# Kernel optimization log

Measured on AMD Instinct MI355X. Metric: run time of the kernel, lower is better.

## Reference

```python
import jax, jax.numpy as jnp
import numpy as np
from jax import lax

NUM_MELS = 80
NQ = 256          # num_quants
WIN = 1024
HOP = 256
K_UP = 800        # upsample kernel
PAD_UP = K_UP + 4 * HOP - WIN   # = 800
RC = 120          # residual_channels
SC = 240          # skip_channels
KC = 2            # causal kernel
NB = 16           # num blocks
DILS = [1, 2, 4, 8, 16, 32, 64, 128] * 2
DN = ('NCH', 'OIH', 'NCH')


def conv1x1(x, w, b):
    # x: [B,C,T], w: [O,C], b: [O]
    return jnp.einsum('bct,oc->bot', x, w) + b[None, :, None]


def causal_conv(x, w, b, d):
    # x: [B,RC,T], w: [2RC,RC,KC], left-pad by d*(KC-1) -> causal, same length
    y = lax.conv_general_dilated(x, w, (1,), [(d * (KC - 1), 0)],
                                 rhs_dilation=(d,), dimension_numbers=DN)
    return y + b[None, :, None]


def setup_inputs() -> dict:
    key = jax.random.key(0)
    ks = jax.random.split(key, 20)
    s = 0.05
    n = jax.random.normal
    return {
        'waveforms': n(ks[0], (1, 40960), jnp.float32),
        'melspecs': n(ks[1], (1, NUM_MELS, 160), jnp.float32),
        # ConvTranspose-equivalent upsample weight, stored as direct conv weight [O,I,K]
        'up_w': s * n(ks[2], (NUM_MELS, NUM_MELS, K_UP), jnp.float32),
        'up_b': jnp.zeros((NUM_MELS,), jnp.float32),
        'in_w': s * n(ks[3], (RC, 1), jnp.float32),
        'in_b': jnp.zeros((RC,), jnp.float32),
        'blk_causal_w': s * n(ks[4], (NB, 2 * RC, RC, KC), jnp.float32),
        'blk_causal_b': jnp.zeros((NB, 2 * RC), jnp.float32),
        'blk_cond_w': s * n(ks[5], (NB, 2 * RC, NUM_MELS), jnp.float32),
        'blk_cond_b': jnp.zeros((NB, 2 * RC), jnp.float32),
        'blk_skip_w': s * n(ks[6], (NB, SC, RC), jnp.float32),
        'blk_skip_b': jnp.zeros((NB, SC), jnp.float32),
        'blk_res_w': s * n(ks[7], (NB, RC, RC), jnp.float32),
        'blk_res_b': jnp.zeros((NB, RC), jnp.float32),
        'h1_w': s * n(ks[8], (NQ, SC), jnp.float32),
        'h1_b': jnp.zeros((NQ,), jnp.float32),
        'h2_w': s * n(ks[9], (NQ, NQ), jnp.float32),
        'h2_b': jnp.zeros((NQ,), jnp.float32),
    }


def _forward(waveforms, melspecs, up_w, up_b, in_w, in_b,
             blk_causal_w, blk_causal_b, blk_cond_w, blk_cond_b,
             blk_skip_w, blk_skip_b, blk_res_w, blk_res_b,
             h1_w, h1_b, h2_w, h2_b):
    # ConvTranspose1d(stride=HOP, padding=PAD_UP) as lhs-dilated conv:
    # out_len = (F-1)*HOP + K_UP - 2*PAD_UP
    cond = lax.conv_general_dilated(
        melspecs, up_w, (1,), [(K_UP - 1 - PAD_UP, K_UP - 1 - PAD_UP)],
        lhs_dilation=(HOP,), dimension_numbers=DN) + up_b[None, :, None]
    L = min(waveforms.shape[-1], cond.shape[-1])
    wav = waveforms[..., :L]
    cond = cond[..., :L]

    res = conv1x1(wav[:, None, :], in_w, in_b)          # [B,RC,L]
    skip_sum = jnp.zeros((res.shape[0], SC, L), res.dtype)
    for i, d in enumerate(DILS):
        z = causal_conv(res, blk_causal_w[i], blk_causal_b[i], d) \
            + conv1x1(cond, blk_cond_w[i], blk_cond_b[i])  # [B,2RC,L]
        h = jnp.tanh(z[:, :RC]) * jax.nn.sigmoid(z[:, RC:])
        skip_sum = skip_sum + conv1x1(h, blk_skip_w[i], blk_skip_b[i])
        res = res + conv1x1(h, blk_res_w[i], blk_res_b[i])

    x = jax.nn.relu(skip_sum)
    x = jax.nn.relu(conv1x1(x, h1_w, h1_b))
    logits = conv1x1(x, h2_w, h2_b)                      # [B,NQ,L]
    return logits


def reference(waveforms, melspecs, up_w, up_b, in_w, in_b,
              blk_causal_w, blk_causal_b, blk_cond_w, blk_cond_b,
              blk_skip_w, blk_skip_b, blk_res_w, blk_res_b,
              h1_w, h1_b, h2_w, h2_b):
    return _forward(waveforms, melspecs, up_w, up_b, in_w, in_b,
                    blk_causal_w, blk_causal_b, blk_cond_w, blk_cond_b,
                    blk_skip_w, blk_skip_b, blk_res_w, blk_res_b,
                    h1_w, h1_b, h2_w, h2_b)
```

## Files before the change

### kernel.cpp

```cpp
#include <hip/hip_runtime.h>

#define L_LEN 39904
#define NT 624
#define RCH 120
#define SCH 240
#define CMEL 80
#define NQO 256
#define NBLK 16
#define KUP 800

typedef unsigned short u16;
typedef __attribute__((ext_vector_type(8))) short short8;
typedef __attribute__((ext_vector_type(4))) float f32x4;

#define MFMA(a, b, c) __builtin_amdgcn_mfma_f32_16x16x32_bf16((a), (b), (c), 0, 0, 0)

__device__ __forceinline__ u16 f2bf(float f) {
    unsigned u = __float_as_uint(f);
    u += 0x7FFFu + ((u >> 16) & 1u);
    return (u16)(u >> 16);
}
__device__ __forceinline__ unsigned pack2(float a, float b) {
    return (unsigned)f2bf(a) | ((unsigned)f2bf(b) << 16);
}
__device__ __forceinline__ float b16tof(u16 h) {
    return __uint_as_float((unsigned)h << 16);
}
__device__ __forceinline__ float gate(float a, float b) {
    float ea = __expf(2.f * a);
    float th = 1.f - 2.f * __builtin_amdgcn_rcpf(ea + 1.f);
    float sg = __builtin_amdgcn_rcpf(1.f + __expf(-b));
    return th * sg;
}

constexpr size_t O_CONDT = 0;
constexpr size_t O_RESA  = O_CONDT + 7023104;
constexpr size_t O_RESB  = O_RESA + 19153920;
constexpr size_t O_SKIP  = O_RESB + 19153920;
constexpr size_t O_ZFRAG = O_SKIP + 19153920;
constexpr size_t O_SKF   = O_ZFRAG + 2621440;
constexpr size_t O_RF    = O_SKF + 1048576;
constexpr size_t O_H1F   = O_RF + 524288;
constexpr size_t O_H2F   = O_H1F + 131072;
constexpr size_t O_UPF   = O_H2F + 131072;
constexpr size_t O_ZB    = O_UPF + 13107200;
constexpr size_t O_SKB   = O_ZB + 16384;

constexpr size_t H2_CONDT = 0;
constexpr size_t H2_RESF  = 7023104;
constexpr size_t H2_BFA   = H2_RESF + 19153920;
constexpr size_t H2_BFB   = H2_BFA + 9576960;
constexpr size_t H2_ZFRAG = H2_BFB + 9576960;
constexpr size_t H2_SKF   = H2_ZFRAG + 2621440;
constexpr size_t H2_RF    = H2_SKF + 1048576;
constexpr size_t H2_H1F   = H2_RF + 524288;
constexpr size_t H2_H2F   = H2_H1F + 131072;
constexpr size_t H2_ZB    = H2_H2F + 131072;
constexpr size_t H2_SKBS  = H2_ZB + 16384;
constexpr size_t H2_HALL  = H2_SKBS + 16384;
constexpr size_t H_BYTES  = (size_t)NBLK * L_LEN * 120 * 2;
constexpr size_t UPF_BYTES = 13107200;
constexpr size_t NEED_H = H2_HALL + (H_BYTES > UPF_BYTES ? H_BYTES : UPF_BYTES);

__global__ void k_prep_zfrag(const float* __restrict__ bc_w, const float* __restrict__ bq_w,
                             u16* __restrict__ dst) {
    int i = blockIdx.x * 256 + threadIdx.x;
    if (i >= NBLK * 10 * 16 * 512) return;
    int jj = i & 7, lane = (i >> 3) & 63, mt = (i >> 9) & 15;
    int rest = i >> 13, ks = rest % 10, blk = rest / 10;
    int m = mt * 16 + (lane & 15);
    int k = ks * 32 + ((lane >> 4) << 3) + jj;
    float v = 0.f;
    if (m < 240) {
        int o = (m & 1) ? (m >> 1) + 120 : (m >> 1);
        if (k < 120)       v = bc_w[((size_t)(blk * 240 + o) * 120 + k) * 2 + 0];
        else if (k < 240)  v = bc_w[((size_t)(blk * 240 + o) * 120 + (k - 120)) * 2 + 1];
        else               v = bq_w[(size_t)(blk * 240 + o) * 80 + (k - 240)];
    }
    dst[i] = f2bf(v);
}
__global__ void k_prep_skfrag(const float* __restrict__ bs_w, u16* __restrict__ dst) {
    int i = blockIdx.x * 256 + threadIdx.x;
    if (i >= NBLK * 4 * 16 * 512) return;
    int jj = i & 7, lane = (i >> 3) & 63, mt = (i >> 9) & 15;
    int rest = i >> 13, ks = rest & 3, blk = rest >> 2;
    int m = mt * 16 + (lane & 15);
    int k = ks * 32 + ((lane >> 4) << 3) + jj;
    float v = (m < 240 && k < 120) ? bs_w[(size_t)(blk * 240 + m) * 120 + k] : 0.f;
    dst[i] = f2bf(v);
}
__global__ void k_prep_rfrag(const float* __restrict__ br_w, u16* __restrict__ dst) {
    int i = blockIdx.x * 256 + threadIdx.x;
    if (i >= NBLK * 4 * 8 * 512) return;
    int jj = i & 7, lane = (i >> 3) & 63, mt = (i >> 9) & 7;
    int rest = i >> 12, ks = rest & 3, blk = rest >> 2;
    int m = mt * 16 + (lane & 15);
    int k = ks * 32 + ((lane >> 4) << 3) + jj;
    float v = (m < 120 && k < 120) ? br_w[(size_t)(blk * 120 + m) * 120 + k] : 0.f;
    dst[i] = f2bf(v);
}
__global__ void k_prep_h1frag(const float* __restrict__ h1_w, u16* __restrict__ dst) {
    int i = blockIdx.x * 256 + threadIdx.x;
    if (i >= 8 * 16 * 512) return;
    int jj = i & 7, lane = (i >> 3) & 63, mt = (i >> 9) & 15, ks = i >> 13;
    int m = mt * 16 + (lane & 15);
    int k = ks * 32 + ((lane >> 4) << 3) + jj;
    float v = (k < 240) ? h1_w[(size_t)m * 240 + k] : 0.f;
    dst[i] = f2bf(v);
}
__global__ void k_prep_h2frag(const float* __restrict__ h2_w, u16* __restrict__ dst) {
    int i = blockIdx.x * 256 + threadIdx.x;
    if (i >= 8 * 16 * 512) return;
    int jj = i & 7, lane = (i >> 3) & 63, mt = (i >> 9) & 15, ks = i >> 13;
    int m = mt * 16 + (lane & 15);
    int k = ks * 32 + ((lane >> 4) << 3) + jj;
    dst[i] = f2bf(h2_w[(size_t)m * 256 + k]);
}
__global__ void k_prep_upfrag(const float* __restrict__ up_w, u16* __restrict__ dst) {
    int i = blockIdx.x * 256 + threadIdx.x;
    if (i >= 256 * 10 * 5 * 512) return;
    int jj = i & 7, lane = (i >> 3) & 63;
    int rest = i >> 9;
    int mt = rest % 5; rest /= 5;
    int ks = rest % 10; int p = rest / 10;
    int m = mt * 16 + (lane & 15);
    int k = ks * 32 + ((lane >> 4) << 3) + jj;
    int c = k >> 2, j = k & 3;
    int r = (256 - ((p + 1) & 255)) & 255;
    int kk = r + 256 * j;
    float v = (m < 80 && kk < KUP) ? up_w[((size_t)m * 80 + c) * KUP + kk] : 0.f;
    dst[i] = f2bf(v);
}
__global__ void k_prep_zbias(const float* __restrict__ bc_b, const float* __restrict__ bq_b,
                             float* __restrict__ dst) {
    int i = blockIdx.x * 256 + threadIdx.x;
    if (i >= NBLK * 256) return;
    int m = i & 255, blk = i >> 8;
    float v = 0.f;
    if (m < 240) {
        int o = (m & 1) ? (m >> 1) + 120 : (m >> 1);
        v = bc_b[blk * 240 + o] + bq_b[blk * 240 + o];
    }
    dst[i] = v;
}
__global__ void k_prep_skbias(const float* __restrict__ bs_b, float* __restrict__ dst) {
    int i = blockIdx.x * 256 + threadIdx.x;
    if (i >= NBLK * 240) return;
    dst[i] = bs_b[i];
}
__global__ void k_prep_skbsum(const float* __restrict__ bs_b, float* __restrict__ dst) {
    int m = blockIdx.x * 256 + threadIdx.x;
    if (m >= 240) return;
    float s = 0.f;
    for (int i = 0; i < NBLK; i++) s += bs_b[i * 240 + m];
    dst[m] = s;
}
__global__ void k_res_initT(const float* __restrict__ wav, const float* __restrict__ in_w,
                            const float* __restrict__ in_b, float* __restrict__ resT) {
    int i = blockIdx.x * 256 + threadIdx.x;
    if (i >= L_LEN * RCH) return;
    int t = i / RCH, c = i % RCH;
    resT[i] = wav[t] * in_w[c] + in_b[c];
}
__global__ void k_res_initT2(const float* __restrict__ wav, const float* __restrict__ in_w,
                             const float* __restrict__ in_b, float* __restrict__ resT,
                             u16* __restrict__ resB) {
    int i = blockIdx.x * 256 + threadIdx.x;
    if (i >= L_LEN * RCH) return;
    int t = i / RCH, c = i % RCH;
    float v = wav[t] * in_w[c] + in_b[c];
    resT[i] = v;
    resB[i] = f2bf(v);
}

__global__ __launch_bounds__(256) void k_up(const float* __restrict__ mel,
        const u16* __restrict__ upf, const float* __restrict__ up_b,
        u16* __restrict__ condT) {
    __shared__ u16 s_ms[64 * 328];
    const int tid = threadIdx.x, l = tid & 63, w = tid >> 6;
    const int quad = l >> 4, tloc = l & 15;
    const int p = blockIdx.x, s0 = blockIdx.y * 64;
    for (int rr = 0; rr < 16; rr++) {
        int tt = w + 4 * rr;
        int sg = s0 + tt;
        #pragma unroll
        for (int base = 0; base < 320; base += 64) {
            int ck = base + l;
            int c = ck >> 2, j = ck & 3;
            int mi = 1 + j + sg;
            float v = (mi < 160) ? mel[c * 160 + mi] : 0.f;
            s_ms[tt * 328 + ck] = f2bf(v);
        }
    }
    __syncthreads();
    f32x4 acc[2][4];
    #pragma unroll
    for (int i = 0; i < 2; i++)
        #pragma unroll
        for (int n = 0; n < 4; n++) acc[i][n] = (f32x4){0.f, 0.f, 0.f, 0.f};
    const int nmt = (w == 0) ? 2 : 1;
    int mts[2]; mts[0] = w; mts[1] = 4;
    for (int ks = 0; ks < 10; ks++) {
        short8 b[4];
        int k0 = ks * 32 + quad * 8;
        #pragma unroll
        for (int n = 0; n < 4; n++)
            b[n] = *(const short8*)&s_ms[(n * 16 + tloc) * 328 + k0];
        const short8* ap = (const short8*)(upf) + ((size_t)p * 10 + ks) * 5 * 64;
        for (int i = 0; i < nmt; i++) {
            short8 a = ap[mts[i] * 64 + l];
            #pragma unroll
            for (int n = 0; n < 4; n++) acc[i][n] = MFMA(a, b[n], acc[i][n]);
        }
    }
    for (int i = 0; i < nmt; i++) {
        int o_base = mts[i] * 16 + quad * 4;
        float4 ub = *(const float4*)(up_b + o_base);
        float bb[4] = {ub.x, ub.y, ub.z, ub.w};
        #pragma unroll
        for (int n = 0; n < 4; n++) {
            int sg = s0 + n * 16 + tloc;
            int t = p + 256 * sg;
            if (t < L_LEN) {
                #pragma unroll
                for (int r = 0; r < 4; r++)
                    condT[(size_t)t * 88 + o_base + r] = f2bf(acc[i][n][r] + bb[r]);
            }
        }
    }
}

__global__ __launch_bounds__(512, 4) void k_block(
        const u16* __restrict__ condT, const float* __restrict__ resT_in,
        float* __restrict__ resT_out, u16* __restrict__ skipT,
        const u16* __restrict__ zfrag, const u16* __restrict__ skfrag,
        const u16* __restrict__ rfrag, const float* __restrict__ zbias,
        const float* __restrict__ skbias, const float* __restrict__ resb,
        int blk, int dil, int first) {
    __shared__ u16 s_x[64 * 328];
    u16* s_h = s_x;
    const int tid = threadIdx.x, l = tid & 63, w = tid >> 6;
    const int quad = l >> 4, tloc = l & 15;
    const int t0 = blockIdx.x * 64;
    const short8* zap = (const short8*)(zfrag) + (size_t)blk * 10 * 16 * 64;
    short8 a_cur[2], a_nxt[2];
    #pragma unroll
    for (int i = 0; i < 2; i++) a_cur[i] = zap[(size_t)(w * 2 + i) * 64 + l];
    for (int rr = 0; rr < 8; rr++) {
        int tt = w + 8 * rr;
        int tg = t0 + tt, tp = tg - dil;
        if (l < 60) {
            float2 pv = make_float2(0.f, 0.f), cv = make_float2(0.f, 0.f);
            if (tp >= 0 && tp < L_LEN) pv = *(const float2*)(resT_in + (size_t)tp * 120 + 2 * l);
            if (tg < L_LEN)            cv = *(const float2*)(resT_in + (size_t)tg * 120 + 2 * l);
            *(unsigned*)&s_x[tt * 328 + 2 * l]       = pack2(pv.x, pv.y);
            *(unsigned*)&s_x[tt * 328 + 120 + 2 * l] = pack2(cv.x, cv.y);
        }
        if (l < 40) {
            unsigned q = 0;
            if (tg < L_LEN) q = *(const unsigned*)(condT + (size_t)tg * 88 + 2 * l);
            *(unsigned*)&s_x[tt * 328 + 240 + 2 * l] = q;
        }
    }
    __syncthreads();
    f32x4 acc[2][4];
    #pragma unroll
    for (int i = 0; i < 2; i++)
        #pragma unroll
        for (int n = 0; n < 4; n++) acc[i][n] = (f32x4){0.f, 0.f, 0.f, 0.f};
    for (int ks = 0; ks < 10; ks++) {
        if (ks < 9) {
            #pragma unroll
            for (int i = 0; i < 2; i++)
                a_nxt[i] = zap[((size_t)(ks + 1) * 16 + w * 2 + i) * 64 + l];
        }
        int k0 = ks * 32 + quad * 8;
        short8 b[4];
        #pragma unroll
        for (int n = 0; n < 4; n++)
            b[n] = *(const short8*)&s_x[(n * 16 + tloc) * 328 + k0];
        #pragma unroll
        for (int i = 0; i < 2; i++)
            #pragma unroll
            for (int n = 0; n < 4; n++) acc[i][n] = MFMA(a_cur[i], b[n], acc[i][n]);
        #pragma unroll
        for (int i = 0; i < 2; i++) a_cur[i] = a_nxt[i];
    }
    const short8* sap = (const short8*)(skfrag) + (size_t)blk * 4 * 16 * 64;
    const short8* rap = (const short8*)(rfrag) + (size_t)blk * 4 * 8 * 64;
    short8 sa_c[2], sa_n[2], ra_c, ra_n;
    #pragma unroll
    for (int i = 0; i < 2; i++) sa_c[i] = sap[(size_t)(w * 2 + i) * 64 + l];
    ra_c = rap[(size_t)w * 64 + l];
    uint2 skp[2][4];
    if (!first) {
        #pragma unroll
        for (int i = 0; i < 2; i++) {
            int m_base = (w * 2 + i) * 16 + quad * 4;
            if (m_base < 240) {
                #pragma unroll
                for (int n = 0; n < 4; n++) {
                    int t = t0 + n * 16 + tloc;
                    if (t < L_LEN)
                        skp[i][n] = *(const uint2*)(skipT + (size_t)t * 240 + m_base);
                }
            }
        }
    }
    unsigned hu[2][4];
    #pragma unroll
    for (int i = 0; i < 2; i++) {
        int m_base = (w * 2 + i) * 16 + quad * 4;
        float4 bz4 = *(const float4*)(zbias + blk * 256 + m_base);
        #pragma unroll
        for (int n = 0; n < 4; n++) {
            float h0 = gate(acc[i][n][0] + bz4.x, acc[i][n][1] + bz4.y);
            float h1 = gate(acc[i][n][2] + bz4.z, acc[i][n][3] + bz4.w);
            hu[i][n] = pack2(h0, h1);
        }
    }
    __syncthreads();
    #pragma unroll
    for (int i = 0; i < 2; i++) {
        int j0 = (w * 2 + i) * 8 + quad * 2;
        #pragma unroll
        for (int n = 0; n < 4; n++)
            *(unsigned*)&s_h[(n * 16 + tloc) * 136 + j0] = hu[i][n];
    }
    __syncthreads();
    f32x4 sacc[2][4], racc[4];
    #pragma unroll
    for (int i = 0; i < 2; i++)
        #pragma unroll
        for (int n = 0; n < 4; n++) sacc[i][n] = (f32x4){0.f, 0.f, 0.f, 0.f};
    #pragma unroll
    for (int n = 0; n < 4; n++) racc[n] = (f32x4){0.f, 0.f, 0.f, 0.f};
    for (int ks = 0; ks < 4; ks++) {
        if (ks < 3) {
            #pragma unroll
            for (int i = 0; i < 2; i++)
                sa_n[i] = sap[((size_t)(ks + 1) * 16 + w * 2 + i) * 64 + l];
            ra_n = rap[((size_t)(ks + 1) * 8 + w) * 64 + l];
        }
        short8 b[4];
        int k0 = ks * 32 + quad * 8;
        #pragma unroll
        for (int n = 0; n < 4; n++)
            b[n] = *(const short8*)&s_h[(n * 16 + tloc) * 136 + k0];
        #pragma unroll
        for (int i = 0; i < 2; i++)
            #pragma unroll
            for (int n = 0; n < 4; n++) sacc[i][n] = MFMA(sa_c[i], b[n], sacc[i][n]);
        #pragma unroll
        for (int n = 0; n < 4; n++) racc[n] = MFMA(ra_c, b[n], racc[n]);
        #pragma unroll
        for (int i = 0; i < 2; i++) sa_c[i] = sa_n[i];
        ra_c = ra_n;
    }
    #pragma unroll
    for (int i = 0; i < 2; i++) {
        int m_base = (w * 2 + i) * 16 + quad * 4;
        if (m_base >= 240) continue;
        float4 sb4 = *(const float4*)(skbias + blk * 240 + m_base);
        #pragma unroll
        for (int n = 0; n < 4; n++) {
            int t = t0 + n * 16 + tloc;
            if (t >= L_LEN) continue;
            float x0 = sacc[i][n][0] + sb4.x;
            float x1 = sacc[i][n][1] + sb4.y;
            float x2 = sacc[i][n][2] + sb4.z;
            float x3 = sacc[i][n][3] + sb4.w;
            if (!first) {
                uint2 pv = skp[i][n];
                x0 += b16tof((u16)(pv.x & 0xFFFF));
                x1 += b16tof((u16)(pv.x >> 16));
                x2 += b16tof((u16)(pv.y & 0xFFFF));
                x3 += b16tof((u16)(pv.y >> 16));
            }
            uint2 ov;
            ov.x = pack2(x0, x1);
            ov.y = pack2(x2, x3);
            *(uint2*)(skipT + (size_t)t * 240 + m_base) = ov;
        }
    }
    {
        int m_base = w * 16 + quad * 4;
        if (m_base < 120) {
            float4 rb4 = *(const float4*)(resb + blk * 120 + m_base);
            #pragma unroll
            for (int n = 0; n < 4; n++) {
                int t = t0 + n * 16 + tloc;
                if (t >= L_LEN) continue;
                float4 cur = *(const float4*)(resT_in + (size_t)t * 120 + m_base);
                float4 o;
                o.x = cur.x + racc[n][0] + rb4.x;
                o.y = cur.y + racc[n][1] + rb4.y;
                o.z = cur.z + racc[n][2] + rb4.z;
                o.w = cur.w + racc[n][3] + rb4.w;
                *(float4*)(resT_out + (size_t)t * 120 + m_base) = o;
            }
        }
    }
}

__global__ __launch_bounds__(512, 4) void k_block_h2(
        const u16* __restrict__ condT, float* __restrict__ resF,
        const u16* __restrict__ bfIn, u16* __restrict__ bfOut,
        u16* __restrict__ hout,
        const u16* __restrict__ zfrag, const u16* __restrict__ rfrag,
        const float* __restrict__ zbias, const float* __restrict__ resb,
        int blk, int dil) {
    __shared__ u16 s_h[64 * 136];
    const int tid = threadIdx.x, l = tid & 63, w = tid >> 6;
    const int quad = l >> 4, tloc = l & 15;
    const int t0 = blockIdx.x * 64;
    const short8 ZV = {0, 0, 0, 0, 0, 0, 0, 0};
    int oP[4], oC[4], oQ[4];
    bool pz[4];
    #pragma unroll
    for (int n = 0; n < 4; n++) {
        int tn = t0 + n * 16 + tloc;
        int tc = tn < L_LEN ? tn : L_LEN - 1;
        int tp = tn - dil;
        pz[n] = (tp < 0);
        int tpc = tp < 0 ? 0 : (tp < L_LEN ? tp : L_LEN - 1);
        oP[n] = tpc * 120;
        oC[n] = tc * 120;
        oQ[n] = tc * 88;
    }
    const short8* zap = (const short8*)(zfrag) + (size_t)blk * 10 * 16 * 64;
    short8 a_cur[2], a_nxt[2];
    a_cur[0] = zap[(size_t)(w * 2 + 0) * 64 + l];
    a_cur[1] = zap[(size_t)(w * 2 + 1) * 64 + l];
    f32x4 acc[2][4];
    #pragma unroll
    for (int i = 0; i < 2; i++)
        #pragma unroll
        for (int n = 0; n < 4; n++) acc[i][n] = (f32x4){0.f, 0.f, 0.f, 0.f};
    short8 bc[4], bn[4];
    {
        int k0 = quad * 8;
        #pragma unroll
        for (int n = 0; n < 4; n++) {
            short8 v = *(const short8*)(bfIn + oP[n] + k0);
            if (pz[n]) v = ZV;
            bc[n] = v;
        }
    }
    #pragma unroll
    for (int ks = 0; ks < 10; ks++) {
        if (ks < 9) {
            int k1 = (ks + 1) * 32 + quad * 8;
            #pragma unroll
            for (int n = 0; n < 4; n++) {
                short8 v;
                if (k1 < 120) {
                    v = *(const short8*)(bfIn + oP[n] + k1);
                    if (pz[n]) v = ZV;
                } else if (k1 < 240) {
                    v = *(const short8*)(bfIn + oC[n] + (k1 - 120));
                } else {
                    v = *(const short8*)(condT + oQ[n] + (k1 - 240));
                }
                bn[n] = v;
            }
            a_nxt[0] = zap[((size_t)(ks + 1) * 16 + w * 2 + 0) * 64 + l];
            a_nxt[1] = zap[((size_t)(ks + 1) * 16 + w * 2 + 1) * 64 + l];
        }
        #pragma unroll
        for (int i = 0; i < 2; i++)
            #pragma unroll
            for (int n = 0; n < 4; n++) acc[i][n] = MFMA(a_cur[i], bc[n], acc[i][n]);
        #pragma unroll
        for (int n = 0; n < 4; n++) bc[n] = bn[n];
        a_cur[0] = a_nxt[0]; a_cur[1] = a_nxt[1];
    }
    const short8* rap = (const short8*)(rfrag) + (size_t)blk * 4 * 8 * 64;
    short8 ra_c = rap[(size_t)w * 64 + l], ra_n;
    const int m_r = w * 16 + quad * 4;
    float4 cur_pf[4] = {};
    if (m_r < 120) {
        #pragma unroll
        for (int n = 0; n < 4; n++) {
            int t = t0 + n * 16 + tloc;
            if (t < L_LEN) cur_pf[n] = *(const float4*)(resF + (size_t)t * 120 + m_r);
        }
    }
    unsigned hu[2][4];
    #pragma unroll
    for (int i = 0; i < 2; i++) {
        int m_base = (w * 2 + i) * 16 + quad * 4;
        float4 bz4 = *(const float4*)(zbias + blk * 256 + m_base);
        #pragma unroll
        for (int n = 0; n < 4; n++) {
            float h0 = gate(acc[i][n][0] + bz4.x, acc[i][n][1] + bz4.y);
            float h1 = gate(acc[i][n][2] + bz4.z, acc[i][n][3] + bz4.w);
            hu[i][n] = pack2(h0, h1);
        }
    }
    #pragma unroll
    for (int i = 0; i < 2; i++) {
        int j0 = (w * 2 + i) * 8 + quad * 2;
        #pragma unroll
        for (int n = 0; n < 4; n++)
            *(unsigned*)&s_h[(n * 16 + tloc) * 136 + j0] = hu[i][n];
    }
    __syncthreads();
    for (int rr = 0; rr < 8; rr++) {
        int tt = w + 8 * rr, tg = t0 + tt;
        if (l < 60 && tg < L_LEN)
            *(unsigned*)&hout[(size_t)tg * 120 + 2 * l] =
                *(const unsigned*)&s_h[tt * 136 + 2 * l];
    }
    f32x4 racc[4];
    #pragma unroll
    for (int n = 0; n < 4; n++) racc[n] = (f32x4){0.f, 0.f, 0.f, 0.f};
    for (int ks = 0; ks < 4; ks++) {
        if (ks < 3) ra_n = rap[((size_t)(ks + 1) * 8 + w) * 64 + l];
        short8 b[4];
        int k0 = ks * 32 + quad * 8;
        #pragma unroll
        for (int n = 0; n < 4; n++)
            b[n] = *(const short8*)&s_h[(n * 16 + tloc) * 136 + k0];
        #pragma unroll
        for (int n = 0; n < 4; n++) racc[n] = MFMA(ra_c, b[n], racc[n]);
        ra_c = ra_n;
    }
    if (m_r < 120) {
        float4 rb4 = *(const float4*)(resb + blk * 120 + m_r);
        #pragma unroll
        for (int n = 0; n < 4; n++) {
            int t = t0 + n * 16 + tloc;
            if (t >= L_LEN) continue;
            float4 o;
            o.x = cur_pf[n].x + racc[n][0] + rb4.x;
            o.y = cur_pf[n].y + racc[n][1] + rb4.y;
            o.z = cur_pf[n].z + racc[n][2] + rb4.z;
            o.w = cur_pf[n].w + racc[n][3] + rb4.w;
            *(float4*)(resF + (size_t)t * 120 + m_r) = o;
            uint2 hv;
            hv.x = pack2(o.x, o.y);
            hv.y = pack2(o.z, o.w);
            *(uint2*)(bfOut + (size_t)t * 120 + m_r) = hv;
        }
    }
}

__global__ __launch_bounds__(512, 4) void k_final(const u16* __restrict__ skipT,
        const u16* __restrict__ h1f, const u16* __restrict__ h2f,
        const float* __restrict__ h1_b, const float* __restrict__ h2_b,
        float* __restrict__ out) {
    __shared__ u16 s_m[64 * 264];
    const int tid = threadIdx.x, l = tid & 63, w = tid >> 6;
    const int quad = l >> 4, tloc = l & 15;
    const int t0 = blockIdx.x * 64;
    const short8* ap1 = (const short8*)h1f;
    short8 a_cur[2], a_nxt[2];
    #pragma unroll
    for (int i = 0; i < 2; i++) a_cur[i] = ap1[(size_t)(w * 2 + i) * 64 + l];
    for (int rr = 0; rr < 8; rr++) {
        int tt = w + 8 * rr;
        int tg = t0 + tt;
        uint2 v = make_uint2(0u, 0u);
        if (l < 60 && tg < L_LEN)
            v = *(const uint2*)(skipT + (size_t)tg * 240 + 4 * l);
        float x0 = fmaxf(b16tof((u16)(v.x & 0xFFFF)), 0.f);
        float x1 = fmaxf(b16tof((u16)(v.x >> 16)), 0.f);
        float x2 = fmaxf(b16tof((u16)(v.y & 0xFFFF)), 0.f);
        float x3 = fmaxf(b16tof((u16)(v.y >> 16)), 0.f);
        uint2 ov;
        ov.x = pack2(x0, x1);
        ov.y = pack2(x2, x3);
        *(uint2*)&s_m[tt * 264 + 4 * l] = ov;
    }
    __syncthreads();
    f32x4 acc[2][4];
    #pragma unroll
    for (int i = 0; i < 2; i++)
        #pragma unroll
        for (int n = 0; n < 4; n++) acc[i][n] = (f32x4){0.f, 0.f, 0.f, 0.f};
    for (int ks = 0; ks < 8; ks++) {
        if (ks < 7) {
            #pragma unroll
            for (int i = 0; i < 2; i++)
                a_nxt[i] = ap1[((size_t)(ks + 1) * 16 + w * 2 + i) * 64 + l];
        }
        short8 b[4];
        int k0 = ks * 32 + quad * 8;
        #pragma unroll
        for (int n = 0; n < 4; n++)
            b[n] = *(const short8*)&s_m[(n * 16 + tloc) * 264 + k0];
        #pragma unroll
        for (int i = 0; i < 2; i++)
            #pragma unroll
            for (int n = 0; n < 4; n++) acc[i][n] = MFMA(a_cur[i], b[n], acc[i][n]);
        #pragma unroll
        for (int i = 0; i < 2; i++) a_cur[i] = a_nxt[i];
    }
    unsigned ylo[2][4], yhi[2][4];
    #pragma unroll
    for (int i = 0; i < 2; i++) {
        int m_base = (w * 2 + i) * 16 + quad * 4;
        float4 b1 = *(const float4*)(h1_b + m_base);
        #pragma unroll
        for (int n = 0; n < 4; n++) {
            float y0 = fmaxf(acc[i][n][0] + b1.x, 0.f);
            float y1v = fmaxf(acc[i][n][1] + b1.y, 0.f);
            float y2 = fmaxf(acc[i][n][2] + b1.z, 0.f);
            float y3 = fmaxf(acc[i][n][3] + b1.w, 0.f);
            ylo[i][n] = pack2(y0, y1v);
            yhi[i][n] = pack2(y2, y3);
        }
    }
    const short8* ap2 = (const short8*)h2f;
    #pragma unroll
    for (int i = 0; i < 2; i++) a_cur[i] = ap2[(size_t)(w * 2 + i) * 64 + l];
    __syncthreads();
    #pragma unroll
    for (int i = 0; i < 2; i++) {
        int m_base = (w * 2 + i) * 16 + quad * 4;
        #pragma unroll
        for (int n = 0; n < 4; n++) {
            int t = n * 16 + tloc;
            *(unsigned*)&s_m[t * 264 + m_base]     = ylo[i][n];
            *(unsigned*)&s_m[t * 264 + m_base + 2] = yhi[i][n];
        }
    }
    __syncthreads();
    #pragma unroll
    for (int i = 0; i < 2; i++)
        #pragma unroll
        for (int n = 0; n < 4; n++) acc[i][n] = (f32x4){0.f, 0.f, 0.f, 0.f};
    for (int ks = 0; ks < 8; ks++) {
        if (ks < 7) {
            #pragma unroll
            for (int i = 0; i < 2; i++)
                a_nxt[i] = ap2[((size_t)(ks + 1) * 16 + w * 2 + i) * 64 + l];
        }
        short8 b[4];
        int k0 = ks * 32 + quad * 8;
        #pragma unroll
        for (int n = 0; n < 4; n++)
            b[n] = *(const short8*)&s_m[(n * 16 + tloc) * 264 + k0];
        #pragma unroll
        for (int i = 0; i < 2; i++)
            #pragma unroll
            for (int n = 0; n < 4; n++) acc[i][n] = MFMA(a_cur[i], b[n], acc[i][n]);
        #pragma unroll
        for (int i = 0; i < 2; i++) a_cur[i] = a_nxt[i];
    }
    #pragma unroll
    for (int i = 0; i < 2; i++) {
        int m_base = (w * 2 + i) * 16 + quad * 4;
        float4 b2 = *(const float4*)(h2_b + m_base);
        float bb[4] = {b2.x, b2.y, b2.z, b2.w};
        #pragma unroll
        for (int n = 0; n < 4; n++) {
            int t = t0 + n * 16 + tloc;
            if (t >= L_LEN) continue;
            #pragma unroll
            for (int r = 0; r < 4; r++)
                out[(size_t)(m_base + r) * L_LEN + t] = acc[i][n][r] + bb[r];
        }
    }
}

__global__ __launch_bounds__(512, 4) void k_final_h2(const u16* __restrict__ hall,
        const u16* __restrict__ skf, const u16* __restrict__ h1f,
        const u16* __restrict__ h2f, const float* __restrict__ skbsum,
        const float* __restrict__ h1_b, const float* __restrict__ h2_b,
        float* __restrict__ out) {
    __shared__ u16 s_m[64 * 264];
    const int tid = threadIdx.x, l = tid & 63, w = tid >> 6;
    const int quad = l >> 4, tloc = l & 15;
    const int t0 = blockIdx.x * 64;
    const short8 ZV = {0, 0, 0, 0, 0, 0, 0, 0};
    int ro[4];
    #pragma unroll
    for (int n = 0; n < 4; n++) {
        int tn = t0 + n * 16 + tloc;
        ro[n] = (tn < L_LEN ? tn : L_LEN - 1) * 120;
    }
    const bool kpad = (quad == 3);
    const int k0q = quad * 8;
    const short8* sap = (const short8*)skf;
    short8 sa_c[2], sa_n[2];
    sa_c[0] = sap[(size_t)(w * 2 + 0) * 64 + l];
    sa_c[1] = sap[(size_t)(w * 2 + 1) * 64 + l];
    f32x4 sacc[2][4];
    #pragma unroll
    for (int i = 0; i < 2; i++)
        #pragma unroll
        for (int n = 0; n < 4; n++) sacc[i][n] = (f32x4){0.f, 0.f, 0.f, 0.f};
    short8 bc[4], bn[4];
    #pragma unroll
    for (int n = 0; n < 4; n++)
        bc[n] = *(const short8*)(hall + ro[n] + k0q);
    for (int g = 0; g < 64; g++) {
        if (g < 63) {
            int g1 = g + 1;
            const u16* hp = hall + (size_t)(g1 >> 2) * ((size_t)L_LEN * 120);
            int kk = (g1 & 3) * 32 + k0q;
            bool pad = ((g1 & 3) == 3) && kpad;
            #pragma unroll
            for (int n = 0; n < 4; n++) {
                short8 v = *(const short8*)(hp + ro[n] + kk);
                if (pad) v = ZV;
                bn[n] = v;
            }
            sa_n[0] = sap[((size_t)g1 * 16 + w * 2 + 0) * 64 + l];
            sa_n[1] = sap[((size_t)g1 * 16 + w * 2 + 1) * 64 + l];
        }
        #pragma unroll
        for (int i2 = 0; i2 < 2; i2++)
            #pragma unroll
            for (int n = 0; n < 4; n++)
                sacc[i2][n] = MFMA(sa_c[i2], bc[n], sacc[i2][n]);
        #pragma unroll
        for (int n = 0; n < 4; n++) bc[n] = bn[n];
        sa_c[0] = sa_n[0]; sa_c[1] = sa_n[1];
    }
    const short8* ap1 = (const short8*)h1f;
    short8 a_cur[2], a_nxt[2];
    a_cur[0] = ap1[(size_t)(w * 2 + 0) * 64 + l];
    a_cur[1] = ap1[(size_t)(w * 2 + 1) * 64 + l];
    #pragma unroll
    for (int i2 = 0; i2 < 2; i2++) {
        int m_base = (w * 2 + i2) * 16 + quad * 4;
        float4 sb4 = make_float4(0.f, 0.f, 0.f, 0.f);
        bool valid = (m_base < 240);
        if (valid) sb4 = *(const float4*)(skbsum + m_base);
        #pragma unroll
        for (int n = 0; n < 4; n++) {
            float x0 = 0.f, x1 = 0.f, x2 = 0.f, x3 = 0.f;
            if (valid) {
                x0 = fmaxf(sacc[i2][n][0] + sb4.x, 0.f);
                x1 = fmaxf(sacc[i2][n][1] + sb4.y, 0.f);
                x2 = fmaxf(sacc[i2][n][2] + sb4.z, 0.f);
                x3 = fmaxf(sacc[i2][n][3] + sb4.w, 0.f);
            }
            int t = n * 16 + tloc;
            *(unsigned*)&s_m[t * 264 + m_base]     = pack2(x0, x1);
            *(unsigned*)&s_m[t * 264 + m_base + 2] = pack2(x2, x3);
        }
    }
    __syncthreads();
    f32x4 acc[2][4];
    #pragma unroll
    for (int i = 0; i < 2; i++)
        #pragma unroll
        for (int n = 0; n < 4; n++) acc[i][n] = (f32x4){0.f, 0.f, 0.f, 0.f};
    for (int ks = 0; ks < 8; ks++) {
        if (ks < 7) {
            #pragma unroll
            for (int i = 0; i < 2; i++)
                a_nxt[i] = ap1[((size_t)(ks + 1) * 16 + w * 2 + i) * 64 + l];
        }
        short8 b[4];
        int k0 = ks * 32 + quad * 8;
        #pragma unroll
        for (int n = 0; n < 4; n++)
            b[n] = *(const short8*)&s_m[(n * 16 + tloc) * 264 + k0];
        #pragma unroll
        for (int i = 0; i < 2; i++)
            #pragma unroll
            for (int n = 0; n < 4; n++) acc[i][n] = MFMA(a_cur[i], b[n], acc[i][n]);
        #pragma unroll
        for (int i = 0; i < 2; i++) a_cur[i] = a_nxt[i];
    }
    unsigned ylo[2][4], yhi[2][4];
    #pragma unroll
    for (int i = 0; i < 2; i++) {
        int m_base = (w * 2 + i) * 16 + quad * 4;
        float4 b1 = *(const float4*)(h1_b + m_base);
        #pragma unroll
        for (int n = 0; n < 4; n++) {
            float y0 = fmaxf(acc[i][n][0] + b1.x, 0.f);
            float y1v = fmaxf(acc[i][n][1] + b1.y, 0.f);
            float y2 = fmaxf(acc[i][n][2] + b1.z, 0.f);
            float y3 = fmaxf(acc[i][n][3] + b1.w, 0.f);
            ylo[i][n] = pack2(y0, y1v);
            yhi[i][n] = pack2(y2, y3);
        }
    }
    const short8* ap2 = (const short8*)h2f;
    #pragma unroll
    for (int i = 0; i < 2; i++) a_cur[i] = ap2[(size_t)(w * 2 + i) * 64 + l];
    __syncthreads();
    #pragma unroll
    for (int i = 0; i < 2; i++) {
        int m_base = (w * 2 + i) * 16 + quad * 4;
        #pragma unroll
        for (int n = 0; n < 4; n++) {
            int t = n * 16 + tloc;
            *(unsigned*)&s_m[t * 264 + m_base]     = ylo[i][n];
            *(unsigned*)&s_m[t * 264 + m_base + 2] = yhi[i][n];
        }
    }
    __syncthreads();
    #pragma unroll
    for (int i = 0; i < 2; i++)
        #pragma unroll
        for (int n = 0; n < 4; n++) acc[i][n] = (f32x4){0.f, 0.f, 0.f, 0.f};
    for (int ks = 0; ks < 8; ks++) {
        if (ks < 7) {
            #pragma unroll
            for (int i = 0; i < 2; i++)
                a_nxt[i] = ap2[((size_t)(ks + 1) * 16 + w * 2 + i) * 64 + l];
        }
        short8 b[4];
        int k0 = ks * 32 + quad * 8;
        #pragma unroll
        for (int n = 0; n < 4; n++)
            b[n] = *(const short8*)&s_m[(n * 16 + tloc) * 264 + k0];
        #pragma unroll
        for (int i = 0; i < 2; i++)
            #pragma unroll
            for (int n = 0; n < 4; n++) acc[i][n] = MFMA(a_cur[i], b[n], acc[i][n]);
        #pragma unroll
        for (int i = 0; i < 2; i++) a_cur[i] = a_nxt[i];
    }
    #pragma unroll
    for (int i = 0; i < 2; i++) {
        int m_base = (w * 2 + i) * 16 + quad * 4;
        float4 b2 = *(const float4*)(h2_b + m_base);
        float bb[4] = {b2.x, b2.y, b2.z, b2.w};
        #pragma unroll
        for (int n = 0; n < 4; n++) {
            int t = t0 + n * 16 + tloc;
            if (t >= L_LEN) continue;
            #pragma unroll
            for (int r = 0; r < 4; r++)
                out[(size_t)(m_base + r) * L_LEN + t] = acc[i][n][r] + bb[r];
        }
    }
}

extern "C" void kernel_launch(void* const* d_in, const int* in_sizes, int n_in,
                              void* d_out, int out_size, void* d_ws, size_t ws_size,
                              hipStream_t stream) {
    const float* wav   = (const float*)d_in[0];
    const float* mel   = (const float*)d_in[1];
    const float* up_w  = (const float*)d_in[2];
    const float* up_b  = (const float*)d_in[3];
    const float* in_w  = (const float*)d_in[4];
    const float* in_b  = (const float*)d_in[5];
    const float* bc_w  = (const float*)d_in[6];
    const float* bc_b  = (const float*)d_in[7];
    const float* bq_w  = (const float*)d_in[8];
    const float* bq_b  = (const float*)d_in[9];
    const float* bs_w  = (const float*)d_in[10];
    const float* bs_b  = (const float*)d_in[11];
    const float* br_w  = (const float*)d_in[12];
    const float* br_b  = (const float*)d_in[13];
    const float* h1_w  = (const float*)d_in[14];
    const float* h1_b  = (const float*)d_in[15];
    const float* h2_w  = (const float*)d_in[16];
    const float* h2_b  = (const float*)d_in[17];

    char* wsb = (char*)d_ws;
    const bool use_h = (ws_size >= NEED_H);

    if (use_h) {
        u16*   condT = (u16*)(wsb + H2_CONDT);
        float* resF  = (float*)(wsb + H2_RESF);
        u16*   bfA   = (u16*)(wsb + H2_BFA);
        u16*   bfB   = (u16*)(wsb + H2_BFB);
        u16*   zfrag = (u16*)(wsb + H2_ZFRAG);
        u16*   skf   = (u16*)(wsb + H2_SKF);
        u16*   rf    = (u16*)(wsb + H2_RF);
        u16*   h1f   = (u16*)(wsb + H2_H1F);
        u16*   h2f   = (u16*)(wsb + H2_H2F);
        float* zb    = (float*)(wsb + H2_ZB);
        float* skbs  = (float*)(wsb + H2_SKBS);
        u16*   hall  = (u16*)(wsb + H2_HALL);
        u16*   upf   = (u16*)(wsb + H2_HALL);

        k_prep_zfrag <<<5120, 256, 0, stream>>>(bc_w, bq_w, zfrag);
        k_prep_skfrag<<<2048, 256, 0, stream>>>(bs_w, skf);
        k_prep_rfrag <<<1024, 256, 0, stream>>>(br_w, rf);
        k_prep_h1frag<<<256, 256, 0, stream>>>(h1_w, h1f);
        k_prep_h2frag<<<256, 256, 0, stream>>>(h2_w, h2f);
        k_prep_upfrag<<<25600, 256, 0, stream>>>(up_w, upf);
        k_prep_zbias <<<16, 256, 0, stream>>>(bc_b, bq_b, zb);
        k_prep_skbsum<<<1, 256, 0, stream>>>(bs_b, skbs);
        k_res_initT2 <<<(L_LEN * RCH + 255) / 256, 256, 0, stream>>>(wav, in_w, in_b, resF, bfA);
        k_up<<<dim3(256, 3), 256, 0, stream>>>(mel, upf, up_b, condT);

        for (int i = 0; i < NBLK; i++) {
            int d = 1 << (i & 7);
            const u16* bfIn = (i & 1) ? bfB : bfA;
            u16* bfOut      = (i & 1) ? bfA : bfB;
            k_block_h2<<<NT, 512, 0, stream>>>(condT, resF, bfIn, bfOut,
                                               hall + (size_t)i * (size_t)L_LEN * 120,
                                               zfrag, rf, zb, br_b, i, d);
        }
        k_final_h2<<<NT, 512, 0, stream>>>(hall, skf, h1f, h2f, skbs, h1_b, h2_b,
                                           (float*)d_out);
    } else {
        u16*   condT = (u16*)(wsb + O_CONDT);
        float* resA  = (float*)(wsb + O_RESA);
        float* resB  = (float*)(wsb + O_RESB);
        u16*   skipT = (u16*)(wsb + O_SKIP);
        u16*   zfrag = (u16*)(wsb + O_ZFRAG);
        u16*   skf   = (u16*)(wsb + O_SKF);
        u16*   rf    = (u16*)(wsb + O_RF);
        u16*   h1f   = (u16*)(wsb + O_H1F);
        u16*   h2f   = (u16*)(wsb + O_H2F);
        u16*   upf   = (u16*)(wsb + O_UPF);
        float* zb    = (float*)(wsb + O_ZB);
        float* skb   = (float*)(wsb + O_SKB);

        k_prep_zfrag <<<5120, 256, 0, stream>>>(bc_w, bq_w, zfrag);
        k_prep_skfrag<<<2048, 256, 0, stream>>>(bs_w, skf);
        k_prep_rfrag <<<1024, 256, 0, stream>>>(br_w, rf);
        k_prep_h1frag<<<256, 256, 0, stream>>>(h1_w, h1f);
        k_prep_h2frag<<<256, 256, 0, stream>>>(h2_w, h2f);
        k_prep_upfrag<<<25600, 256, 0, stream>>>(up_w, upf);
        k_prep_zbias <<<16, 256, 0, stream>>>(bc_b, bq_b, zb);
        k_prep_skbias<<<15, 256, 0, stream>>>(bs_b, skb);
        k_res_initT  <<<(L_LEN * RCH + 255) / 256, 256, 0, stream>>>(wav, in_w, in_b, resA);
        k_up<<<dim3(256, 3), 256, 0, stream>>>(mel, upf, up_b, condT);

        for (int i = 0; i < NBLK; i++) {
            int d = 1 << (i & 7);
            const float* rin = (i & 1) ? resB : resA;
            float* rout      = (i & 1) ? resA : resB;
            k_block<<<NT, 512, 0, stream>>>(condT, rin, rout, skipT, zfrag, skf, rf,
                                            zb, skb, br_b, i, d, (i == 0) ? 1 : 0);
        }
        k_final<<<NT, 512, 0, stream>>>(skipT, h1f, h2f, h1_b, h2_b, (float*)d_out);
    }
}
```

Before: 804.7 us.

## Stage block inputs and final-stage hidden tiles in LDS with double buffering

The per-block kernel now loads the current residual, the dilated previous rows and the conditioning into shared memory once per tile. Where the dilation is smaller than the tile, the shifted rows are copied within LDS instead of being re-read from global memory. MFMA B operands then come from LDS instead of scattered per-lane global short8 loads. The final kernel double-buffers each block's gated activations through LDS with register prefetch, which replaces the per-MFMA global gathers. The cost is extra synchronisation and larger shared-memory use, which may lower occupancy.

```diff
diff --git a/kernel.cpp b/kernel.cpp
--- a/kernel.cpp
+++ b/kernel.cpp
@@ -403,76 +403,69 @@
     }
 }
 
-__global__ __launch_bounds__(512, 4) void k_block_h2(
+__global__ __launch_bounds__(512, 4) void k_block_h3(
         const u16* __restrict__ condT, float* __restrict__ resF,
         const u16* __restrict__ bfIn, u16* __restrict__ bfOut,
         u16* __restrict__ hout,
         const u16* __restrict__ zfrag, const u16* __restrict__ rfrag,
         const float* __restrict__ zbias, const float* __restrict__ resb,
         int blk, int dil) {
-    __shared__ u16 s_h[64 * 136];
+    __shared__ u16 s_x[64 * 328];
+    u16* s_h = s_x;
     const int tid = threadIdx.x, l = tid & 63, w = tid >> 6;
     const int quad = l >> 4, tloc = l & 15;
     const int t0 = blockIdx.x * 64;
-    const short8 ZV = {0, 0, 0, 0, 0, 0, 0, 0};
-    int oP[4], oC[4], oQ[4];
-    bool pz[4];
-    #pragma unroll
-    for (int n = 0; n < 4; n++) {
-        int tn = t0 + n * 16 + tloc;
-        int tc = tn < L_LEN ? tn : L_LEN - 1;
-        int tp = tn - dil;
-        pz[n] = (tp < 0);
-        int tpc = tp < 0 ? 0 : (tp < L_LEN ? tp : L_LEN - 1);
-        oP[n] = tpc * 120;
-        oC[n] = tc * 120;
-        oQ[n] = tc * 88;
-    }
     const short8* zap = (const short8*)(zfrag) + (size_t)blk * 10 * 16 * 64;
     short8 a_cur[2], a_nxt[2];
     a_cur[0] = zap[(size_t)(w * 2 + 0) * 64 + l];
     a_cur[1] = zap[(size_t)(w * 2 + 1) * 64 + l];
+    const uint2 Z2 = make_uint2(0u, 0u);
+    for (int rr = 0; rr < 8; rr++) {
+        int tt = w + 8 * rr, tg = t0 + tt;
+        if (l < 30) {
+            uint2 cv = (tg < L_LEN) ? *(const uint2*)(bfIn + (size_t)tg * 120 + 4 * l) : Z2;
+            *(uint2*)&s_x[tt * 328 + 120 + 4 * l] = cv;
+            if (tt < dil) {
+                int tp = tg - dil;
+                uint2 pv = (tp >= 0 && tp < L_LEN)
+                    ? *(const uint2*)(bfIn + (size_t)tp * 120 + 4 * l) : Z2;
+                *(uint2*)&s_x[tt * 328 + 4 * l] = pv;
+            }
+        } else if (l >= 32 && l < 54) {
+            int c = l - 32;
+            uint2 q = (tg < L_LEN) ? *(const uint2*)(condT + (size_t)tg * 88 + 4 * c) : Z2;
+            *(uint2*)&s_x[tt * 328 + 240 + 4 * c] = q;
+        }
+    }
+    __syncthreads();
+    if (dil < 64) {
+        for (int rr = 0; rr < 8; rr++) {
+            int tt = w + 8 * rr;
+            if (l < 30 && tt >= dil)
+                *(uint2*)&s_x[tt * 328 + 4 * l] =
+                    *(const uint2*)&s_x[(tt - dil) * 328 + 120 + 4 * l];
+        }
+        __syncthreads();
+    }
     f32x4 acc[2][4];
     #pragma unroll
     for (int i = 0; i < 2; i++)
         #pragma unroll
         for (int n = 0; n < 4; n++) acc[i][n] = (f32x4){0.f, 0.f, 0.f, 0.f};
-    short8 bc[4], bn[4];
-    {
-        int k0 = quad * 8;
-        #pragma unroll
-        for (int n = 0; n < 4; n++) {
-            short8 v = *(const short8*)(bfIn + oP[n] + k0);
-            if (pz[n]) v = ZV;
-            bc[n] = v;
-        }
-    }
-    #pragma unroll
     for (int ks = 0; ks < 10; ks++) {
         if (ks < 9) {
-            int k1 = (ks + 1) * 32 + quad * 8;
-            #pragma unroll
-            for (int n = 0; n < 4; n++) {
-                short8 v;
-                if (k1 < 120) {
-                    v = *(const short8*)(bfIn + oP[n] + k1);
-                    if (pz[n]) v = ZV;
-                } else if (k1 < 240) {
-                    v = *(const short8*)(bfIn + oC[n] + (k1 - 120));
-                } else {
-                    v = *(const short8*)(condT + oQ[n] + (k1 - 240));
-                }
-                bn[n] = v;
-            }
             a_nxt[0] = zap[((size_t)(ks + 1) * 16 + w * 2 + 0) * 64 + l];
             a_nxt[1] = zap[((size_t)(ks + 1) * 16 + w * 2 + 1) * 64 + l];
         }
+        int k0 = ks * 32 + quad * 8;
+        short8 b[4];
+        #pragma unroll
+        for (int n = 0; n < 4; n++)
+            b[n] = *(const short8*)&s_x[(n * 16 + tloc) * 328 + k0];
         #pragma unroll
         for (int i = 0; i < 2; i++)
             #pragma unroll
-            for (int n = 0; n < 4; n++) acc[i][n] = MFMA(a_cur[i], bc[n], acc[i][n]);
-        #pragma unroll
-        for (int n = 0; n < 4; n++) bc[n] = bn[n];
+            for (int n = 0; n < 4; n++) acc[i][n] = MFMA(a_cur[i], b[n], acc[i][n]);
         a_cur[0] = a_nxt[0]; a_cur[1] = a_nxt[1];
     }
     const short8* rap = (const short8*)(rfrag) + (size_t)blk * 4 * 8 * 64;
@@ -498,6 +491,7 @@
             hu[i][n] = pack2(h0, h1);
         }
     }
+    __syncthreads();
     #pragma unroll
     for (int i = 0; i < 2; i++) {
         int j0 = (w * 2 + i) * 8 + quad * 2;
@@ -665,25 +659,41 @@
     }
 }
 
-__global__ __launch_bounds__(512, 4) void k_final_h2(const u16* __restrict__ hall,
+__global__ __launch_bounds__(512, 4) void k_final_h3(const u16* __restrict__ hall,
         const u16* __restrict__ skf, const u16* __restrict__ h1f,
         const u16* __restrict__ h2f, const float* __restrict__ skbsum,
         const float* __restrict__ h1_b, const float* __restrict__ h2_b,
         float* __restrict__ out) {
-    __shared__ u16 s_m[64 * 264];
+    __shared__ u16 smem[2 * 64 * 136];
+    u16* s_m = smem;
     const int tid = threadIdx.x, l = tid & 63, w = tid >> 6;
     const int quad = l >> 4, tloc = l & 15;
     const int t0 = blockIdx.x * 64;
-    const short8 ZV = {0, 0, 0, 0, 0, 0, 0, 0};
-    int ro[4];
-    #pragma unroll
-    for (int n = 0; n < 4; n++) {
-        int tn = t0 + n * 16 + tloc;
-        ro[n] = (tn < L_LEN ? tn : L_LEN - 1) * 120;
-    }
-    const bool kpad = (quad == 3);
-    const int k0q = quad * 8;
     const short8* sap = (const short8*)skf;
+
+    unsigned ha[8], hb[8];
+    auto LOADH = [&](unsigned (&reg)[8], int i) {
+        const u16* hp = hall + (size_t)i * ((size_t)L_LEN * 120);
+        #pragma unroll
+        for (int rr = 0; rr < 8; rr++) {
+            int tg = t0 + w + 8 * rr;
+            reg[rr] = (l < 60 && tg < L_LEN)
+                ? *(const unsigned*)&hp[(size_t)tg * 120 + 2 * l] : 0u;
+        }
+    };
+    if (l >= 60) {
+        #pragma unroll
+        for (int rr = 0; rr < 8; rr++) {
+            int row = w + 8 * rr;
+            *(unsigned*)&smem[row * 136 + 2 * l] = 0u;
+            *(unsigned*)&smem[64 * 136 + row * 136 + 2 * l] = 0u;
+        }
+    }
+    LOADH(ha, 0);
+    #pragma unroll
+    for (int rr = 0; rr < 8; rr++)
+        if (l < 60) *(unsigned*)&smem[(w + 8 * rr) * 136 + 2 * l] = ha[rr];
+    LOADH(hb, 1);
     short8 sa_c[2], sa_n[2];
     sa_c[0] = sap[(size_t)(w * 2 + 0) * 64 + l];
     sa_c[1] = sap[(size_t)(w * 2 + 1) * 64 + l];
@@ -692,33 +702,38 @@
     for (int i = 0; i < 2; i++)
         #pragma unroll
         for (int n = 0; n < 4; n++) sacc[i][n] = (f32x4){0.f, 0.f, 0.f, 0.f};
-    short8 bc[4], bn[4];
-    #pragma unroll
-    for (int n = 0; n < 4; n++)
-        bc[n] = *(const short8*)(hall + ro[n] + k0q);
-    for (int g = 0; g < 64; g++) {
-        if (g < 63) {
-            int g1 = g + 1;
-            const u16* hp = hall + (size_t)(g1 >> 2) * ((size_t)L_LEN * 120);
-            int kk = (g1 & 3) * 32 + k0q;
-            bool pad = ((g1 & 3) == 3) && kpad;
-            #pragma unroll
-            for (int n = 0; n < 4; n++) {
-                short8 v = *(const short8*)(hp + ro[n] + kk);
-                if (pad) v = ZV;
-                bn[n] = v;
+    __syncthreads();
+    #pragma unroll
+    for (int i = 0; i < 16; i++) {
+        u16* cur = smem + (i & 1) * (64 * 136);
+        u16* nxt = smem + ((i + 1) & 1) * (64 * 136);
+        unsigned (&wrg)[8] = (i & 1) ? ha : hb;
+        unsigned (&lrg)[8] = (i & 1) ? hb : ha;
+        if (i < 15) {
+            #pragma unroll
+            for (int rr = 0; rr < 8; rr++)
+                if (l < 60) *(unsigned*)&nxt[(w + 8 * rr) * 136 + 2 * l] = wrg[rr];
+        }
+        if (i < 14) LOADH(lrg, i + 2);
+        for (int ks = 0; ks < 4; ks++) {
+            int g = i * 4 + ks;
+            if (g < 63) {
+                sa_n[0] = sap[((size_t)(g + 1) * 16 + w * 2 + 0) * 64 + l];
+                sa_n[1] = sap[((size_t)(g + 1) * 16 + w * 2 + 1) * 64 + l];
             }
-            sa_n[0] = sap[((size_t)g1 * 16 + w * 2 + 0) * 64 + l];
-            sa_n[1] = sap[((size_t)g1 * 16 + w * 2 + 1) * 64 + l];
-        }
-        #pragma unroll
-        for (int i2 = 0; i2 < 2; i2++)
+            int k0 = ks * 32 + quad * 8;
+            short8 b[4];
             #pragma unroll
             for (int n = 0; n < 4; n++)
-                sacc[i2][n] = MFMA(sa_c[i2], bc[n], sacc[i2][n]);
-        #pragma unroll
-        for (int n = 0; n < 4; n++) bc[n] = bn[n];
-        sa_c[0] = sa_n[0]; sa_c[1] = sa_n[1];
+                b[n] = *(const short8*)&cur[(n * 16 + tloc) * 136 + k0];
+            #pragma unroll
+            for (int i2 = 0; i2 < 2; i2++)
+                #pragma unroll
+                for (int n = 0; n < 4; n++)
+                    sacc[i2][n] = MFMA(sa_c[i2], b[n], sacc[i2][n]);
+            sa_c[0] = sa_n[0]; sa_c[1] = sa_n[1];
+        }
+        __syncthreads();
     }
     const short8* ap1 = (const short8*)h1f;
     short8 a_cur[2], a_nxt[2];
@@ -891,11 +906,11 @@
             int d = 1 << (i & 7);
             const u16* bfIn = (i & 1) ? bfB : bfA;
             u16* bfOut      = (i & 1) ? bfA : bfB;
-            k_block_h2<<<NT, 512, 0, stream>>>(condT, resF, bfIn, bfOut,
+            k_block_h3<<<NT, 512, 0, stream>>>(condT, resF, bfIn, bfOut,
                                                hall + (size_t)i * (size_t)L_LEN * 120,
                                                zfrag, rf, zb, br_b, i, d);
         }
-        k_final_h2<<<NT, 512, 0, stream>>>(hall, skf, h1f, h2f, skbs, h1_b, h2_b,
+        k_final_h3<<<NT, 512, 0, stream>>>(hall, skf, h1f, h2f, skbs, h1_b, h2_b,
                                            (float*)d_out);
     } else {
         u16*   condT = (u16*)(wsb + O_CONDT);
```

Result: faster. 783.2 us (-2.7%).
